# Performance work log

Hardware: AMD Instinct MI355X
Metric: run time of the kernel (lower is better)

Reference implementation:

```python
import jax, jax.numpy as jnp
import numpy as np

T_ITERS = 48  # number of unrolled PDHG iterations (init kwarg T)


def _grad3(u):
    """Forward-difference gradient with circular BC.
    u: (P, 1, X, Y, T) -> (P, 3, X, Y, T).
    conv with kernel (0,-1,1) + circular pad == roll(v,-1,axis) - v."""
    v = u[:, 0]
    return jnp.stack([jnp.roll(v, -1, axis=a) - v for a in (1, 2, 3)], axis=1)


def _grad3_adj(q):
    """Adjoint (negative divergence) with circular BC.
    q: (P, 3, X, Y, T) -> (P, 1, X, Y, T)."""
    out = sum(jnp.roll(q[:, d], 1, axis=d + 1) - q[:, d] for d in range(3))
    return out[:, None]


def setup_inputs() -> dict:
    key = jax.random.key(0)
    k1, k2 = jax.random.split(key)
    x = jax.random.normal(k1, (2, 1, 160, 160, 16), dtype=jnp.float32)
    # positive per-voxel regularization map, one per gradient direction
    lambda_map = jax.random.uniform(k2, (2, 3, 160, 160, 16), dtype=jnp.float32)
    return {"x": x, "lambda_map": lambda_map}


def reference(x, lambda_map):
    # op_norm_AHA = 1, op_norm_GHG = sqrt(12) -> L = sqrt(1 + 12)
    L = jnp.sqrt(jnp.asarray(13.0, x.dtype))
    s10 = jax.nn.sigmoid(jnp.asarray(10.0, x.dtype))  # sigmoid of init value 10.0
    sigma = s10 / L
    tau = s10 / L
    theta = s10

    xnoisy = x
    p = x
    q = jnp.zeros((x.shape[0], 3) + x.shape[2:], dtype=x.dtype)
    x0 = x
    xbar = x

    def step(carry, _):
        p, q, x0, xbar = carry
        p = (p + sigma * (xbar - xnoisy)) / (1.0 + sigma)
        q = jnp.clip(q + sigma * _grad3(xbar), -lambda_map, lambda_map)
        x1 = x0 - tau * p - tau * _grad3_adj(q)
        xbar = x1 + theta * (x1 - x0)
        return (p, q, x1, xbar), None

    (p, q, x1, xbar), _ = jax.lax.scan(step, (p, q, x0, xbar), None, length=T_ITERS)
    return x1
```

## Files before the change

kernel.cpp:

```cpp
#include <hip/hip_runtime.h>
#include <math.h>

#define XDIM 160
#define YDIM 160
#define TDIM 16
#define NB 2
#define T_ITERS 48
#define TILE 10
#define R1S 16
#define R0S 18
#define TPT (XDIM / TILE)
#define NTHR 512

constexpr int VOL  = XDIM * YDIM * TDIM;
constexpr int NX   = NB * VOL;
constexpr int NBLK = NB * TPT * TPT;

typedef _Float16 hreal;
typedef _Float16 half4 __attribute__((ext_vector_type(4)));

__device__ __forceinline__ float clampl(float v, float l) {
    return fminf(fmaxf(v, -l), l);
}
__device__ __forceinline__ int wrap(int v) {
    return v < 0 ? v + XDIM : (v >= XDIM ? v - XDIM : v);
}
__device__ __forceinline__ void ld4(const float* p, float* d) {
    float4 v = *(const float4*)p;
    d[0] = v.x; d[1] = v.y; d[2] = v.z; d[3] = v.w;
}
__device__ __forceinline__ void st4(float* p, const float* s) {
    *(float4*)p = make_float4(s[0], s[1], s[2], s[3]);
}
__device__ __forceinline__ void h2f4(const hreal* p, float* d) {
    half4 v = *(const half4*)p;
    d[0] = (float)v.x; d[1] = (float)v.y; d[2] = (float)v.z; d[3] = (float)v.w;
}

__global__ __launch_bounds__(256) void init_kernel(
    const float* __restrict__ x, const float* __restrict__ lam,
    float* __restrict__ pA, float* __restrict__ xA,
    hreal* __restrict__ xbAh, hreal* __restrict__ qAh,
    hreal* __restrict__ lamh, hreal* __restrict__ xnh)
{
    int i = blockIdx.x * blockDim.x + threadIdx.x;
    if (i < NX) {
        float v = x[i];
        pA[i] = v; xA[i] = v;
        xbAh[i] = (hreal)v;
        xnh[i]  = (hreal)v;
    }
    if (i < 3 * NX) {
        qAh[i]  = (hreal)0.f;
        lamh[i] = (hreal)lam[i];
    }
}

__global__ __launch_bounds__(NTHR, 4) void pd_step4(
    const hreal* __restrict__ xnh, const hreal* __restrict__ lamh,
    const float* __restrict__ pIn, float* __restrict__ pOut,
    const float* __restrict__ xIn, float* __restrict__ xOut,
    const hreal* __restrict__ xbIn, hreal* __restrict__ xbOut,
    const hreal* __restrict__ qIn, hreal* __restrict__ qOut,
    float sigma, float inv1ps, float tau, float theta)
{
    __shared__ float xbS[R0S * R0S * TDIM];
    __shared__ float q0S[(R1S + 1) * R1S * TDIM];
    __shared__ float q1S[R1S * (R1S + 1) * TDIM];

    const int tid = threadIdx.x;
    const int b   = blockIdx.x / (TPT * TPT);
    const int rem = blockIdx.x % (TPT * TPT);
    const int X0  = (rem / TPT) * TILE;
    const int Y0  = (rem % TPT) * TILE;
    const int xbase = b * VOL, qbase = b * 3 * VOL;

    const int qd = tid & 3, t0 = qd * 4;
    const int lane  = tid & 63;
    const int upSrc = (lane & 60) | ((lane + 1) & 3);
    const int dnSrc = (lane & 60) | ((lane + 3) & 3);

    for (int s = tid; s < R0S * R0S * 4; s += NTHR) {
        int sq = s & 3, ln = s >> 2;
        int rx = ln / R0S, ry = ln % R0S;
        int gx = wrap(X0 - 4 + rx), gy = wrap(Y0 - 4 + ry);
        float v[4];
        h2f4(xbIn + xbase + (gx * YDIM + gy) * TDIM + sq * 4, v);
        st4(xbS + ln * TDIM + sq * 4, v);
    }
    for (int s = tid; s < 17 * 16 * 4; s += NTHR) {
        int sq = s & 3, ln = s >> 2;
        int sx = ln / 16, sy = ln % 16;
        int gx = wrap(X0 - 4 + sx), gy = wrap(Y0 - 3 + sy);
        float v[4];
        h2f4(qIn + qbase + (gx * YDIM + gy) * TDIM + sq * 4, v);
        st4(q0S + ln * TDIM + sq * 4, v);
    }
    for (int s = tid; s < 16 * 17 * 4; s += NTHR) {
        int sq = s & 3, ln = s >> 2;
        int sx = ln / 17, sy = ln % 17;
        int gx = wrap(X0 - 3 + sx), gy = wrap(Y0 - 4 + sy);
        float v[4];
        h2f4(qIn + qbase + VOL + (gx * YDIM + gy) * TDIM + sq * 4, v);
        st4(q1S + ln * TDIM + sq * 4, v);
    }

    float p[2][4], xv[2][4], xb[2][4], q0[2][4], q1[2][4], q2[2][4];
    half4 XNr[2], L0r[2], L1r[2], L2r[2];
    #pragma unroll
    for (int m = 0; m < 2; ++m) {
        int line = 128 * m + (tid >> 2);
        int lx = line >> 4, ly = line & 15;
        int gx = wrap(X0 - 3 + lx), gy = wrap(Y0 - 3 + ly);
        int off  = xbase + (gx * YDIM + gy) * TDIM + t0;
        int qoff = qbase + (gx * YDIM + gy) * TDIM + t0;
        ld4(pIn + off, p[m]);
        ld4(xIn + off, xv[m]);
        h2f4(qIn + qoff + 2 * VOL, q2[m]);
        XNr[m] = *(const half4*)(xnh + off);
        L0r[m] = *(const half4*)(lamh + qoff);
        L1r[m] = *(const half4*)(lamh + qoff + VOL);
        L2r[m] = *(const half4*)(lamh + qoff + 2 * VOL);
    }

    half4 LRr;
    if (tid < 64) {
        int rly = tid >> 2;
        LRr = *(const half4*)(lamh + qbase +
              (wrap(X0 - 4) * YDIM + wrap(Y0 - 3 + rly)) * TDIM + t0);
    } else if (tid < 128) {
        int rlx = (tid - 64) >> 2;
        LRr = *(const half4*)(lamh + qbase + VOL +
              (wrap(X0 - 3 + rlx) * YDIM + wrap(Y0 - 4)) * TDIM + t0);
    }

    __syncthreads();

    #pragma unroll
    for (int m = 0; m < 2; ++m) {
        int line = 128 * m + (tid >> 2);
        int lx = line >> 4, ly = line & 15;
        ld4(xbS + ((lx + 1) * R0S + (ly + 1)) * TDIM + t0, xb[m]);
    }

    #pragma unroll
    for (int k = 1; k <= 4; ++k) {
        const int lo = k - 1, hi = 17 - k;

        if (k == 1) {
            if (tid < 64) {
                int rly = tid >> 2;
                float qr[4], xbc[4], xpx[4];
                ld4(q0S + (0 * R1S + rly) * TDIM + t0, qr);
                ld4(xbS + (0 * R0S + (rly + 1)) * TDIM + t0, xbc);
                ld4(xbS + (1 * R0S + (rly + 1)) * TDIM + t0, xpx);
                #pragma unroll
                for (int j = 0; j < 4; ++j)
                    qr[j] = clampl(qr[j] + sigma * (xpx[j] - xbc[j]), (float)LRr[j]);
                st4(q0S + (0 * R1S + rly) * TDIM + t0, qr);
            } else if (tid < 128) {
                int rlx = (tid - 64) >> 2;
                float qr[4], xbc[4], xpy[4];
                ld4(q1S + (rlx * 17 + 0) * TDIM + t0, qr);
                ld4(xbS + ((rlx + 1) * R0S + 0) * TDIM + t0, xbc);
                ld4(xbS + ((rlx + 1) * R0S + 1) * TDIM + t0, xpy);
                #pragma unroll
                for (int j = 0; j < 4; ++j)
                    qr[j] = clampl(qr[j] + sigma * (xpy[j] - xbc[j]), (float)LRr[j]);
                st4(q1S + (rlx * 17 + 0) * TDIM + t0, qr);
            }
        }

        #pragma unroll
        for (int m = 0; m < 2; ++m) {
            int line = 128 * m + (tid >> 2);
            int lx = line >> 4, ly = line & 15;
            bool inX = (lx >= lo && lx < hi), inY = (ly >= lo && ly < hi);
            bool aq0 = inY && (lx >= lo - 1) && (lx < hi);
            bool aq1 = inX && (ly >= lo - 1) && (ly < hi);
            bool ax  = inX && inY;

            if (k == 1) {
                ld4(q0S + ((lx + 1) * R1S + ly) * TDIM + t0, q0[m]);
                ld4(q1S + (lx * 17 + (ly + 1)) * TDIM + t0, q1[m]);
            }
            if (aq0) {
                float xpx[4];
                ld4(xbS + ((lx + 2) * R0S + (ly + 1)) * TDIM + t0, xpx);
                #pragma unroll
                for (int j = 0; j < 4; ++j)
                    q0[m][j] = clampl(q0[m][j] + sigma * (xpx[j] - xb[m][j]),
                                      (float)L0r[m][j]);
                st4(q0S + ((lx + 1) * R1S + ly) * TDIM + t0, q0[m]);
            }
            if (aq1) {
                float xpy[4];
                ld4(xbS + ((lx + 1) * R0S + (ly + 2)) * TDIM + t0, xpy);
                #pragma unroll
                for (int j = 0; j < 4; ++j)
                    q1[m][j] = clampl(q1[m][j] + sigma * (xpy[j] - xb[m][j]),
                                      (float)L1r[m][j]);
                st4(q1S + (lx * 17 + (ly + 1)) * TDIM + t0, q1[m]);
            }
            if (ax) {
                float xb_tp = __shfl(xb[m][0], upSrc, 64);
                #pragma unroll
                for (int j = 0; j < 4; ++j) {
                    float gt = ((j < 3) ? xb[m][j + 1] : xb_tp) - xb[m][j];
                    q2[m][j] = clampl(q2[m][j] + sigma * gt, (float)L2r[m][j]);
                    p[m][j]  = (p[m][j] + sigma * (xb[m][j] - (float)XNr[m][j]))
                               * inv1ps;
                }
            }
        }
        __syncthreads();

        #pragma unroll
        for (int m = 0; m < 2; ++m) {
            int line = 128 * m + (tid >> 2);
            int lx = line >> 4, ly = line & 15;
            bool ax = (lx >= lo && lx < hi && ly >= lo && ly < hi);
            if (ax) {
                float q0b[4], q1b[4];
                ld4(q0S + (lx * R1S + ly) * TDIM + t0, q0b);
                ld4(q1S + (lx * 17 + ly) * TDIM + t0, q1b);
                float q2tm = __shfl(q2[m][3], dnSrc, 64);
                #pragma unroll
                for (int j = 0; j < 4; ++j) {
                    float q2p = (j == 0) ? q2tm : q2[m][j - 1];
                    float div = (q0b[j] - q0[m][j]) + (q1b[j] - q1[m][j])
                              + (q2p - q2[m][j]);
                    float xnew = xv[m][j] - tau * (p[m][j] + div);
                    xb[m][j] = xnew + theta * (xnew - xv[m][j]);
                    xv[m][j] = xnew;
                }
                if (k < 4)
                    st4(xbS + ((lx + 1) * R0S + (ly + 1)) * TDIM + t0, xb[m]);
            }
        }
        if (k < 4) __syncthreads();
    }

    #pragma unroll
    for (int m = 0; m < 2; ++m) {
        int line = 128 * m + (tid >> 2);
        int lx = line >> 4, ly = line & 15;
        if (lx >= 3 && lx < 13 && ly >= 3 && ly < 13) {
            int gx = X0 + lx - 3, gy = Y0 + ly - 3;
            int off  = xbase + (gx * YDIM + gy) * TDIM + t0;
            int qoff = qbase + (gx * YDIM + gy) * TDIM + t0;
            st4(pOut + off, p[m]);
            st4(xOut + off, xv[m]);
            half4 h;
            h.x = (hreal)xb[m][0]; h.y = (hreal)xb[m][1];
            h.z = (hreal)xb[m][2]; h.w = (hreal)xb[m][3];
            *(half4*)(xbOut + off) = h;
            h.x = (hreal)q0[m][0]; h.y = (hreal)q0[m][1];
            h.z = (hreal)q0[m][2]; h.w = (hreal)q0[m][3];
            *(half4*)(qOut + qoff) = h;
            h.x = (hreal)q1[m][0]; h.y = (hreal)q1[m][1];
            h.z = (hreal)q1[m][2]; h.w = (hreal)q1[m][3];
            *(half4*)(qOut + qoff + VOL) = h;
            h.x = (hreal)q2[m][0]; h.y = (hreal)q2[m][1];
            h.z = (hreal)q2[m][2]; h.w = (hreal)q2[m][3];
            *(half4*)(qOut + qoff + 2 * VOL) = h;
        }
    }
}

extern "C" void kernel_launch(void* const* d_in, const int* in_sizes, int n_in,
                              void* d_out, int out_size, void* d_ws, size_t ws_size,
                              hipStream_t stream) {
    const float* x   = (const float*)d_in[0];
    const float* lam = (const float*)d_in[1];
    float* out = (float*)d_out;
    float* ws  = (float*)d_ws;

    float* pA  = ws;
    float* pB  = ws + (size_t)NX;
    float* xBb = ws + (size_t)2 * NX;
    float* xAb = out;
    hreal* hb  = (hreal*)(ws + (size_t)3 * NX);
    hreal* xbAh = hb;
    hreal* xbBh = hb + (size_t)NX;
    hreal* qAh  = hb + (size_t)2 * NX;
    hreal* qBh  = hb + (size_t)5 * NX;
    hreal* lamh = hb + (size_t)8 * NX;
    hreal* xnh  = hb + (size_t)11 * NX;

    const double s10 = 1.0 / (1.0 + exp(-10.0));
    const double L   = sqrt(13.0);
    float sigma  = (float)(s10 / L);
    float tau    = sigma;
    float theta  = (float)s10;
    float inv1ps = (float)(1.0 / (1.0 + s10 / L));

    init_kernel<<<(3 * NX + 255) / 256, 256, 0, stream>>>(
        x, lam, pA, xAb, xbAh, qAh, lamh, xnh);

    for (int j = 0; j < T_ITERS / 4; ++j) {
        const bool e = (j & 1) == 0;
        pd_step4<<<NBLK, NTHR, 0, stream>>>(
            xnh, lamh,
            e ? pA : pB,   e ? pB : pA,
            e ? xAb : xBb, e ? xBb : xAb,
            e ? xbAh : xbBh, e ? xbBh : xbAh,
            e ? qAh : qBh,  e ? qBh : qAh,
            sigma, inv1ps, tau, theta);
    }
}
```

Measured before the change: 251.3 us.

## Fuse iteration groups into persistent kernel with hierarchical grid barrier

Replaces the 12 separate per-group kernel launches with one persistent kernel. A two-level atomic grid barrier separates the groups. Each block keeps its tile's interior state (p, x, xbar, q) in registers across groups, so only the halo is reloaded from global memory. Lambda and the noisy image are cached in registers once. The time-axis neighbour shifts use DPP lane rotations. The approach needs all 512 blocks to be co-resident, which is checked through the occupancy API with a fallback to the launch loop. It risks barrier spin cost and, if residency is insufficient, deadlock.

```diff
diff --git a/kernel.cpp b/kernel.cpp
--- a/kernel.cpp
+++ b/kernel.cpp
@@ -11,6 +11,8 @@
 #define R0S 18
 #define TPT (XDIM / TILE)
 #define NTHR 512
+#define NGRP (T_ITERS / 4)
+#define NLEAF 8
 
 constexpr int VOL  = XDIM * YDIM * TDIM;
 constexpr int NX   = NB * VOL;
@@ -35,13 +37,56 @@
 __device__ __forceinline__ void h2f4(const hreal* p, float* d) {
     half4 v = *(const half4*)p;
     d[0] = (float)v.x; d[1] = (float)v.y; d[2] = (float)v.z; d[3] = (float)v.w;
+}
+__device__ __forceinline__ float qrot_up(float x) {
+    return __int_as_float(__builtin_amdgcn_update_dpp(
+        0, __float_as_int(x), 0x39, 0xF, 0xF, true));
+}
+__device__ __forceinline__ float qrot_dn(float x) {
+    return __int_as_float(__builtin_amdgcn_update_dpp(
+        0, __float_as_int(x), 0x93, 0xF, 0xF, true));
+}
+
+__device__ __forceinline__ void grid_barrier(unsigned* bar) {
+    __threadfence();
+    __syncthreads();
+    if (threadIdx.x == 0) {
+        unsigned s = __hip_atomic_load(bar + 129, __ATOMIC_RELAXED,
+                                       __HIP_MEMORY_SCOPE_AGENT);
+        const unsigned leaf = (blockIdx.x & (NLEAF - 1)) * 16;
+        const unsigned per  = NBLK / NLEAF;
+        bool done = false;
+        if (__hip_atomic_fetch_add(bar + leaf, 1u, __ATOMIC_ACQ_REL,
+                                   __HIP_MEMORY_SCOPE_AGENT) == per - 1u) {
+            __hip_atomic_store(bar + leaf, 0u, __ATOMIC_RELAXED,
+                               __HIP_MEMORY_SCOPE_AGENT);
+            if (__hip_atomic_fetch_add(bar + 128, 1u, __ATOMIC_ACQ_REL,
+                                       __HIP_MEMORY_SCOPE_AGENT) == NLEAF - 1u) {
+                __hip_atomic_store(bar + 128, 0u, __ATOMIC_RELAXED,
+                                   __HIP_MEMORY_SCOPE_AGENT);
+                __hip_atomic_store(bar + 129, s + 1u, __ATOMIC_RELEASE,
+                                   __HIP_MEMORY_SCOPE_AGENT);
+                done = true;
+            }
+        }
+        if (!done) {
+            for (unsigned it = 0; it < (1u << 22); ++it) {
+                if (__hip_atomic_load(bar + 129, __ATOMIC_RELAXED,
+                                      __HIP_MEMORY_SCOPE_AGENT) != s) break;
+                __builtin_amdgcn_s_sleep(4);
+            }
+        }
+    }
+    __syncthreads();
+    __threadfence();
 }
 
 __global__ __launch_bounds__(256) void init_kernel(
     const float* __restrict__ x, const float* __restrict__ lam,
     float* __restrict__ pA, float* __restrict__ xA,
     hreal* __restrict__ xbAh, hreal* __restrict__ qAh,
-    hreal* __restrict__ lamh, hreal* __restrict__ xnh)
+    hreal* __restrict__ lamh, hreal* __restrict__ xnh,
+    unsigned* __restrict__ bar)
 {
     int i = blockIdx.x * blockDim.x + threadIdx.x;
     if (i < NX) {
@@ -53,6 +98,249 @@
     if (i < 3 * NX) {
         qAh[i]  = (hreal)0.f;
         lamh[i] = (hreal)lam[i];
+    }
+    if (bar && i < 130) bar[i] = 0u;
+}
+
+__global__ __launch_bounds__(NTHR, 4) void pd_persist(
+    const hreal* __restrict__ xnh, const hreal* __restrict__ lamh,
+    float* __restrict__ pA, float* __restrict__ pB,
+    float* __restrict__ xA, float* __restrict__ xB,
+    hreal* __restrict__ xbA, hreal* __restrict__ xbB,
+    hreal* __restrict__ qA, hreal* __restrict__ qB,
+    unsigned* __restrict__ bar,
+    float sigma, float inv1ps, float tau, float theta)
+{
+    __shared__ float xbS[R0S * R0S * TDIM];
+    __shared__ float q0S[(R1S + 1) * R1S * TDIM];
+    __shared__ float q1S[R1S * (R1S + 1) * TDIM];
+
+    const int tid = threadIdx.x;
+    const int b   = blockIdx.x / (TPT * TPT);
+    const int rem = blockIdx.x % (TPT * TPT);
+    const int X0  = (rem / TPT) * TILE;
+    const int Y0  = (rem % TPT) * TILE;
+    const int xbase = b * VOL, qbase = b * 3 * VOL;
+    const int t0 = (tid & 3) * 4;
+
+    float p[2][4], xv[2][4], xb[2][4], q0[2][4], q1[2][4], q2[2][4];
+    half4 XNr[2], L0r[2], L1r[2], L2r[2];
+
+    #pragma unroll
+    for (int m = 0; m < 2; ++m) {
+        int line = 128 * m + (tid >> 2);
+        int lx = line >> 4, ly = line & 15;
+        int gx = wrap(X0 - 3 + lx), gy = wrap(Y0 - 3 + ly);
+        int off  = xbase + (gx * YDIM + gy) * TDIM + t0;
+        int qoff = qbase + (gx * YDIM + gy) * TDIM + t0;
+        XNr[m] = *(const half4*)(xnh + off);
+        L0r[m] = *(const half4*)(lamh + qoff);
+        L1r[m] = *(const half4*)(lamh + qoff + VOL);
+        L2r[m] = *(const half4*)(lamh + qoff + 2 * VOL);
+    }
+    half4 LRr;
+    if (tid < 64) {
+        int rly = tid >> 2;
+        LRr = *(const half4*)(lamh + qbase +
+              (wrap(X0 - 4) * YDIM + wrap(Y0 - 3 + rly)) * TDIM + t0);
+    } else if (tid < 128) {
+        int rlx = (tid - 64) >> 2;
+        LRr = *(const half4*)(lamh + qbase + VOL +
+              (wrap(X0 - 3 + rlx) * YDIM + wrap(Y0 - 4)) * TDIM + t0);
+    }
+
+    #pragma unroll 1
+    for (int g = 0; g < NGRP; ++g) {
+        const bool e = (g & 1) == 0;
+        const bool first = (g == 0);
+        const float* __restrict__ pIn  = e ? pA : pB;
+        float* __restrict__ pOut       = e ? pB : pA;
+        const float* __restrict__ xIn  = e ? xA : xB;
+        float* __restrict__ xOut       = e ? xB : xA;
+        const hreal* __restrict__ xbIn = e ? xbA : xbB;
+        hreal* __restrict__ xbOut      = e ? xbB : xbA;
+        const hreal* __restrict__ qIn  = e ? qA : qB;
+        hreal* __restrict__ qOut       = e ? qB : qA;
+
+        for (int s = tid; s < R0S * R0S * 4; s += NTHR) {
+            int sq = s & 3, ln = s >> 2;
+            int rx = ln / R0S, ry = ln % R0S;
+            if (!first && rx >= 4 && rx < 14 && ry >= 4 && ry < 14) continue;
+            int gx = wrap(X0 - 4 + rx), gy = wrap(Y0 - 4 + ry);
+            float v[4];
+            h2f4(xbIn + xbase + (gx * YDIM + gy) * TDIM + sq * 4, v);
+            st4(xbS + ln * TDIM + sq * 4, v);
+        }
+        for (int s = tid; s < 17 * 16 * 4; s += NTHR) {
+            int sq = s & 3, ln = s >> 2;
+            int sx = ln / 16, sy = ln % 16;
+            if (!first && sx >= 3 && sx < 14 && sy >= 3 && sy < 13) continue;
+            int gx = wrap(X0 - 4 + sx), gy = wrap(Y0 - 3 + sy);
+            float v[4];
+            h2f4(qIn + qbase + (gx * YDIM + gy) * TDIM + sq * 4, v);
+            st4(q0S + ln * TDIM + sq * 4, v);
+        }
+        for (int s = tid; s < 16 * 17 * 4; s += NTHR) {
+            int sq = s & 3, ln = s >> 2;
+            int sx = ln / 17, sy = ln % 17;
+            if (!first && sx >= 3 && sx < 13 && sy >= 3 && sy < 14) continue;
+            int gx = wrap(X0 - 3 + sx), gy = wrap(Y0 - 4 + sy);
+            float v[4];
+            h2f4(qIn + qbase + VOL + (gx * YDIM + gy) * TDIM + sq * 4, v);
+            st4(q1S + ln * TDIM + sq * 4, v);
+        }
+
+        #pragma unroll
+        for (int m = 0; m < 2; ++m) {
+            int line = 128 * m + (tid >> 2);
+            int lx = line >> 4, ly = line & 15;
+            bool c = lx >= 3 && lx < 13 && ly >= 3 && ly < 13;
+            if (first || !c) {
+                int gx = wrap(X0 - 3 + lx), gy = wrap(Y0 - 3 + ly);
+                int off  = xbase + (gx * YDIM + gy) * TDIM + t0;
+                int qoff = qbase + (gx * YDIM + gy) * TDIM + t0;
+                ld4(pIn + off, p[m]);
+                ld4(xIn + off, xv[m]);
+                h2f4(qIn + qoff + 2 * VOL, q2[m]);
+            }
+        }
+        __syncthreads();
+        #pragma unroll
+        for (int m = 0; m < 2; ++m) {
+            int line = 128 * m + (tid >> 2);
+            int lx = line >> 4, ly = line & 15;
+            bool c = lx >= 3 && lx < 13 && ly >= 3 && ly < 13;
+            if (first || !c)
+                ld4(xbS + ((lx + 1) * R0S + (ly + 1)) * TDIM + t0, xb[m]);
+        }
+
+        #pragma unroll
+        for (int k = 1; k <= 4; ++k) {
+            const int lo = k - 1, hi = 17 - k;
+
+            if (k == 1) {
+                if (tid < 64) {
+                    int rly = tid >> 2;
+                    float qr[4], xbc[4], xpx[4];
+                    ld4(q0S + (0 * R1S + rly) * TDIM + t0, qr);
+                    ld4(xbS + (0 * R0S + (rly + 1)) * TDIM + t0, xbc);
+                    ld4(xbS + (1 * R0S + (rly + 1)) * TDIM + t0, xpx);
+                    #pragma unroll
+                    for (int j = 0; j < 4; ++j)
+                        qr[j] = clampl(qr[j] + sigma * (xpx[j] - xbc[j]), (float)LRr[j]);
+                    st4(q0S + (0 * R1S + rly) * TDIM + t0, qr);
+                } else if (tid < 128) {
+                    int rlx = (tid - 64) >> 2;
+                    float qr[4], xbc[4], xpy[4];
+                    ld4(q1S + (rlx * 17 + 0) * TDIM + t0, qr);
+                    ld4(xbS + ((rlx + 1) * R0S + 0) * TDIM + t0, xbc);
+                    ld4(xbS + ((rlx + 1) * R0S + 1) * TDIM + t0, xpy);
+                    #pragma unroll
+                    for (int j = 0; j < 4; ++j)
+                        qr[j] = clampl(qr[j] + sigma * (xpy[j] - xbc[j]), (float)LRr[j]);
+                    st4(q1S + (rlx * 17 + 0) * TDIM + t0, qr);
+                }
+            }
+
+            #pragma unroll
+            for (int m = 0; m < 2; ++m) {
+                int line = 128 * m + (tid >> 2);
+                int lx = line >> 4, ly = line & 15;
+                bool inX = (lx >= lo && lx < hi), inY = (ly >= lo && ly < hi);
+                bool aq0 = inY && (lx >= lo - 1) && (lx < hi);
+                bool aq1 = inX && (ly >= lo - 1) && (ly < hi);
+                bool ax  = inX && inY;
+
+                if (k == 1) {
+                    bool c = lx >= 3 && lx < 13 && ly >= 3 && ly < 13;
+                    if (first || !c) {
+                        ld4(q0S + ((lx + 1) * R1S + ly) * TDIM + t0, q0[m]);
+                        ld4(q1S + (lx * 17 + (ly + 1)) * TDIM + t0, q1[m]);
+                    }
+                }
+                if (aq0) {
+                    float xpx[4];
+                    ld4(xbS + ((lx + 2) * R0S + (ly + 1)) * TDIM + t0, xpx);
+                    #pragma unroll
+                    for (int j = 0; j < 4; ++j)
+                        q0[m][j] = clampl(q0[m][j] + sigma * (xpx[j] - xb[m][j]),
+                                          (float)L0r[m][j]);
+                    st4(q0S + ((lx + 1) * R1S + ly) * TDIM + t0, q0[m]);
+                }
+                if (aq1) {
+                    float xpy[4];
+                    ld4(xbS + ((lx + 1) * R0S + (ly + 2)) * TDIM + t0, xpy);
+                    #pragma unroll
+                    for (int j = 0; j < 4; ++j)
+                        q1[m][j] = clampl(q1[m][j] + sigma * (xpy[j] - xb[m][j]),
+                                          (float)L1r[m][j]);
+                    st4(q1S + (lx * 17 + (ly + 1)) * TDIM + t0, q1[m]);
+                }
+                if (ax) {
+                    float xb_tp = qrot_up(xb[m][0]);
+                    #pragma unroll
+                    for (int j = 0; j < 4; ++j) {
+                        float gt = ((j < 3) ? xb[m][j + 1] : xb_tp) - xb[m][j];
+                        q2[m][j] = clampl(q2[m][j] + sigma * gt, (float)L2r[m][j]);
+                        p[m][j]  = (p[m][j] + sigma * (xb[m][j] - (float)XNr[m][j]))
+                                   * inv1ps;
+                    }
+                }
+            }
+            __syncthreads();
+
+            #pragma unroll
+            for (int m = 0; m < 2; ++m) {
+                int line = 128 * m + (tid >> 2);
+                int lx = line >> 4, ly = line & 15;
+                bool ax = (lx >= lo && lx < hi && ly >= lo && ly < hi);
+                if (ax) {
+                    float q0b[4], q1b[4];
+                    ld4(q0S + (lx * R1S + ly) * TDIM + t0, q0b);
+                    ld4(q1S + (lx * 17 + ly) * TDIM + t0, q1b);
+                    float q2tm = qrot_dn(q2[m][3]);
+                    #pragma unroll
+                    for (int j = 0; j < 4; ++j) {
+                        float q2p = (j == 0) ? q2tm : q2[m][j - 1];
+                        float div = (q0b[j] - q0[m][j]) + (q1b[j] - q1[m][j])
+                                  + (q2p - q2[m][j]);
+                        float xnew = xv[m][j] - tau * (p[m][j] + div);
+                        xb[m][j] = xnew + theta * (xnew - xv[m][j]);
+                        xv[m][j] = xnew;
+                    }
+                    st4(xbS + ((lx + 1) * R0S + (ly + 1)) * TDIM + t0, xb[m]);
+                }
+            }
+            if (k < 4) __syncthreads();
+        }
+
+        #pragma unroll
+        for (int m = 0; m < 2; ++m) {
+            int line = 128 * m + (tid >> 2);
+            int lx = line >> 4, ly = line & 15;
+            if (lx >= 3 && lx < 13 && ly >= 3 && ly < 13) {
+                int gx = X0 + lx - 3, gy = Y0 + ly - 3;
+                int off  = xbase + (gx * YDIM + gy) * TDIM + t0;
+                int qoff = qbase + (gx * YDIM + gy) * TDIM + t0;
+                st4(pOut + off, p[m]);
+                st4(xOut + off, xv[m]);
+                half4 h;
+                h.x = (hreal)xb[m][0]; h.y = (hreal)xb[m][1];
+                h.z = (hreal)xb[m][2]; h.w = (hreal)xb[m][3];
+                *(half4*)(xbOut + off) = h;
+                h.x = (hreal)q0[m][0]; h.y = (hreal)q0[m][1];
+                h.z = (hreal)q0[m][2]; h.w = (hreal)q0[m][3];
+                *(half4*)(qOut + qoff) = h;
+                h.x = (hreal)q1[m][0]; h.y = (hreal)q1[m][1];
+                h.z = (hreal)q1[m][2]; h.w = (hreal)q1[m][3];
+                *(half4*)(qOut + qoff + VOL) = h;
+                h.x = (hreal)q2[m][0]; h.y = (hreal)q2[m][1];
+                h.z = (hreal)q2[m][2]; h.w = (hreal)q2[m][3];
+                *(half4*)(qOut + qoff + 2 * VOL) = h;
+            }
+        }
+
+        if (g + 1 < NGRP) grid_barrier(bar);
     }
 }
 
@@ -287,6 +575,9 @@
     hreal* qBh  = hb + (size_t)5 * NX;
     hreal* lamh = hb + (size_t)8 * NX;
     hreal* xnh  = hb + (size_t)11 * NX;
+    unsigned* bar = (unsigned*)(ws + (size_t)9 * NX);
+
+    const size_t ws_need = (size_t)9 * NX * sizeof(float) + 130 * sizeof(unsigned);
 
     const double s10 = 1.0 / (1.0 + exp(-10.0));
     const double L   = sqrt(13.0);
@@ -295,17 +586,33 @@
     float theta  = (float)s10;
     float inv1ps = (float)(1.0 / (1.0 + s10 / L));
 
+    static int persist_ok = -1;
+    if (persist_ok < 0) {
+        int nb = 0;
+        hipError_t oe = hipOccupancyMaxActiveBlocksPerMultiprocessor(
+            &nb, pd_persist, NTHR, 0);
+        persist_ok = (oe == hipSuccess && nb >= 2) ? 1 : 0;
+        (void)hipGetLastError();
+    }
+    const bool use_persist = persist_ok == 1 && ws_size >= ws_need;
+
     init_kernel<<<(3 * NX + 255) / 256, 256, 0, stream>>>(
-        x, lam, pA, xAb, xbAh, qAh, lamh, xnh);
-
-    for (int j = 0; j < T_ITERS / 4; ++j) {
-        const bool e = (j & 1) == 0;
-        pd_step4<<<NBLK, NTHR, 0, stream>>>(
-            xnh, lamh,
-            e ? pA : pB,   e ? pB : pA,
-            e ? xAb : xBb, e ? xBb : xAb,
-            e ? xbAh : xbBh, e ? xbBh : xbAh,
-            e ? qAh : qBh,  e ? qBh : qAh,
+        x, lam, pA, xAb, xbAh, qAh, lamh, xnh, use_persist ? bar : nullptr);
+
+    if (use_persist) {
+        pd_persist<<<NBLK, NTHR, 0, stream>>>(
+            xnh, lamh, pA, pB, xAb, xBb, xbAh, xbBh, qAh, qBh, bar,
             sigma, inv1ps, tau, theta);
-    }
-}
+    } else {
+        for (int j = 0; j < NGRP; ++j) {
+            const bool e = (j & 1) == 0;
+            pd_step4<<<NBLK, NTHR, 0, stream>>>(
+                xnh, lamh,
+                e ? pA : pB,   e ? pB : pA,
+                e ? xAb : xBb, e ? xBb : xAb,
+                e ? xbAh : xbBh, e ? xbBh : xbAh,
+                e ? qAh : qBh,  e ? qBh : qAh,
+                sigma, inv1ps, tau, theta);
+        }
+    }
+}
```

Measured after the change: 254.5 us. About the same (+1.3%).
